# Optimization experiments

Hardware: AMD Instinct MI355X
Metric: run time of the kernel (lower is better)

Reference implementation:

```python
import jax, jax.numpy as jnp
import numpy as np

B, S, H, P, D = 4, 2048, 2048, 4096, 1024
I = min(1024, P)  # intermediate_dim


def setup_inputs() -> dict:
    key = jax.random.key(0)
    ks = jax.random.split(key, 8)
    sc = lambda n: 1.0 / np.sqrt(n)
    return {
        "x": jax.random.normal(ks[0], (B, S, H), jnp.float32),
        "tensor_pool": jax.random.normal(ks[1], (P, D), jnp.float32),
        "top_k": 2,
        "w1": jax.random.normal(ks[2], (H, I), jnp.float32) * sc(H),
        "b1": jnp.zeros((I,), jnp.float32),
        "w2": jax.random.normal(ks[3], (I, P), jnp.float32) * sc(I),
        "b2": jnp.zeros((P,), jnp.float32),
        "temperature": jnp.float32(0.5),
        "wp": jax.random.normal(ks[4], (H, D), jnp.float32) * sc(H),
        "bp": jnp.zeros((D,), jnp.float32),
        "gamma": jnp.ones((D,), jnp.float32),
        "beta": jnp.zeros((D,), jnp.float32),
        "wm": jax.random.normal(ks[5], (2 * D, D), jnp.float32) * sc(2 * D),
        "bm": jnp.zeros((D,), jnp.float32),
    }


def _layer_norm(h, gamma, beta, eps=1e-5):
    mu = jnp.mean(h, axis=-1, keepdims=True)
    var = jnp.mean(jnp.square(h - mu), axis=-1, keepdims=True)
    return (h - mu) * jax.lax.rsqrt(var + eps) * gamma + beta


def reference(x, tensor_pool, top_k, w1, b1, w2, b2, temperature, wp, bp, gamma, beta, wm, bm):
    pool_size = tensor_pool.shape[0]
    # router MLP
    inter = jax.nn.relu(jnp.einsum('bsh,hi->bsi', x, w1) + b1)
    logits = jnp.einsum('bsi,ip->bsp', inter, w2) + b2
    temp = jnp.clip(temperature, 0.1, 5.0)
    scaled_logits = jnp.clip(logits / temp, -10.0, 10.0)
    # top-k select + softmax over selected
    topk_logits, topk_idx = jax.lax.top_k(scaled_logits, top_k)  # [B,S,K]
    topk_w = jax.nn.softmax(topk_logits, axis=-1)
    # gather pool entries and combine
    experts_out = tensor_pool[topk_idx]                     # [B,S,K,D]
    weighted_map = jnp.einsum('bsk,bskd->bsd', topk_w, experts_out)
    projected_x = _layer_norm(jnp.einsum('bsh,hd->bsd', x, wp) + bp, gamma, beta)
    combined = jnp.concatenate([projected_x, weighted_map], axis=-1)  # [B,S,2D]
    transformation = jnp.einsum('bse,ed->bsd', combined, wm) + bm
    # usage stats via scatter-add
    usage = jnp.zeros((pool_size,), x.dtype).at[topk_idx.reshape(-1)].add(topk_w.reshape(-1))
    usage_fraction = usage / (usage.sum() + 1e-8)
    uniform = 1.0 / pool_size
    scale = min(1.0, x.size / (pool_size * top_k))
    diversity_loss = jnp.mean(jnp.square(usage_fraction - uniform)) * scale * 0.01
    return transformation, diversity_loss
```

## Files before the change

### kernel.cpp

```cpp
#include <hip/hip_runtime.h>
#include <hip/hip_bf16.h>
#include <float.h>
#include <limits.h>

#define NTOK 8192
#define H_   2048
#define P_   4096
#define D_   1024
#define I_   1024

#define MAXC  16
#define DELTA 0.09375f
#define TAU   4.0e-4f
#define FLAGCAP 512

typedef unsigned short ushort_t;
typedef __attribute__((ext_vector_type(8))) short short8;
typedef __attribute__((ext_vector_type(4))) float floatx4;

static __device__ inline ushort_t f2bf(float f) {
    __hip_bfloat16 h = __float2bfloat16(f);
    return *reinterpret_cast<ushort_t*>(&h);
}
static __device__ inline short f2bfs(float f) {
    __hip_bfloat16 h = __float2bfloat16(f);
    return *reinterpret_cast<short*>(&h);
}
static __device__ inline float bf2f(ushort_t s) { return __uint_as_float((unsigned)s << 16); }

static __device__ inline void ins2(float& v0, int& i0, float& v1, int& i1, float v, int i) {
    if (v > v0 || (v == v0 && i < i0)) { v1 = v0; i1 = i0; v0 = v; i0 = i; }
    else if (v > v1 || (v == v1 && i < i1)) { v1 = v; i1 = i; }
}

static __device__ __forceinline__ void gload16(const void* g, void* l) {
    __builtin_amdgcn_global_load_lds(
        (const __attribute__((address_space(1))) unsigned int*)g,
        (__attribute__((address_space(3))) unsigned int*)l,
        16, 0, 0);
}

__global__ __launch_bounds__(256) void prep_weights(
    const float* __restrict__ w2, float* __restrict__ w2tf, ushort_t* __restrict__ w2t,
    const float* __restrict__ wp, ushort_t* __restrict__ wpt,
    const float* __restrict__ wm, ushort_t* __restrict__ wmt,
    const float* __restrict__ w1, ushort_t* __restrict__ w1tHi, ushort_t* __restrict__ w1tLo)
{
    __shared__ float tile[32][33];
    const int tid = threadIdx.x;
    const int tx = tid & 31, ty = tid >> 5;
    int b = blockIdx.x;
    const float* in; int R, Cc, seg, bx, by;
    if (b < 4096)      { seg = 0; in = w2; R = I_; Cc = P_; bx = b & 127; by = b >> 7; }
    else if (b < 6144) { seg = 1; b -= 4096; in = wp; R = H_; Cc = D_; bx = b & 31; by = b >> 5; }
    else if (b < 8192) { seg = 2; b -= 6144; in = wm; R = H_; Cc = D_; bx = b & 31; by = b >> 5; }
    else               { seg = 3; b -= 8192; in = w1; R = H_; Cc = I_; bx = b & 31; by = b >> 5; }
    const int c0 = bx * 32, r0 = by * 32;
#pragma unroll
    for (int j = 0; j < 4; j++)
        tile[ty + j * 8][tx] = in[(size_t)(r0 + ty + j * 8) * Cc + c0 + tx];
    __syncthreads();
#pragma unroll
    for (int j = 0; j < 4; j++) {
        float v = tile[tx][ty + j * 8];
        const size_t o = (size_t)(c0 + ty + j * 8) * R + r0 + tx;
        if (seg == 0)      { w2t[o] = f2bf(v); w2tf[o] = v; }
        else if (seg == 1) { wpt[o] = f2bf(v); }
        else if (seg == 2) { wmt[o] = f2bf(v); }
        else { ushort_t h = f2bf(v); w1tHi[o] = h; w1tLo[o] = f2bf(v - bf2f(h)); }
    }
}

template<int ASRC, int EPI>
__global__ __launch_bounds__(256) void gemm_lds(
    const void* __restrict__ Av, int lda,
    const ushort_t* __restrict__ Bt, int ldb,
    const float* __restrict__ bias,
    float* __restrict__ Cf, ushort_t* __restrict__ Cb, int ldc, int K)
{
    __shared__ ushort_t sA[128 * 32];
    __shared__ ushort_t sB[128 * 32];

    const int tid  = threadIdx.x;
    const int wave = tid >> 6, lane = tid & 63;
    const int lr = lane & 15, lq = lane >> 4;

    const int nwg = gridDim.x * gridDim.y;
    int bid = blockIdx.y * gridDim.x + blockIdx.x;
    bid = (bid & 7) * (nwg >> 3) + (bid >> 3);
    const int bx = bid % gridDim.x, by = bid / gridDim.x;
    const int m0 = by * 128, n0 = bx * 128;
    const int m0w = m0 + (wave >> 1) * 64, n0w = n0 + (wave & 1) * 64;

    const int n1 = tid, n2 = tid + 256;

    floatx4 acc[4][4] = {};

    for (int k0 = 0; k0 < K; k0 += 32) {
        __syncthreads();
        gload16(Bt + (size_t)(n0 + (n1 >> 2)) * ldb + k0 + (n1 & 3) * 8, &sB[n1 * 8]);
        gload16(Bt + (size_t)(n0 + (n2 >> 2)) * ldb + k0 + (n2 & 3) * 8, &sB[n2 * 8]);
        if (ASRC == 1) {
            const ushort_t* Ab = (const ushort_t*)Av;
            gload16(Ab + (size_t)(m0 + (n1 >> 2)) * lda + k0 + (n1 & 3) * 8, &sA[n1 * 8]);
            gload16(Ab + (size_t)(m0 + (n2 >> 2)) * lda + k0 + (n2 & 3) * 8, &sA[n2 * 8]);
        } else {
#pragma unroll
            for (int ss = 0; ss < 2; ss++) {
                const int s = tid + ss * 256;
                const float* ap = (const float*)Av + (size_t)(m0 + (s >> 2)) * lda + k0 + (s & 3) * 8;
                float4 v0 = *(const float4*)ap;
                float4 v1 = *(const float4*)(ap + 4);
                short8 h;
                h[0] = f2bfs(v0.x); h[1] = f2bfs(v0.y); h[2] = f2bfs(v0.z); h[3] = f2bfs(v0.w);
                h[4] = f2bfs(v1.x); h[5] = f2bfs(v1.y); h[6] = f2bfs(v1.z); h[7] = f2bfs(v1.w);
                *(short8*)&sA[s * 8] = h;
            }
        }
        __syncthreads();

        short8 aF[4], bF[4];
#pragma unroll
        for (int f = 0; f < 4; f++) {
            const int ra = ((wave >> 1) * 64 + f * 16 + lr) * 32 + lq * 8;
            aF[f] = *(const short8*)&sA[ra];
            const int rb = ((wave & 1) * 64 + f * 16 + lr) * 32 + lq * 8;
            bF[f] = *(const short8*)&sB[rb];
        }
#pragma unroll
        for (int i = 0; i < 4; i++)
#pragma unroll
            for (int j = 0; j < 4; j++)
                acc[i][j] = __builtin_amdgcn_mfma_f32_16x16x32_bf16(aF[i], bF[j], acc[i][j], 0, 0, 0);
    }

#pragma unroll
    for (int j = 0; j < 4; j++) {
        const int col = n0w + j * 16 + lr;
        const float bv = bias[col];
#pragma unroll
        for (int i = 0; i < 4; i++) {
            const int rowb = m0w + i * 16 + lq * 4;
#pragma unroll
            for (int r = 0; r < 4; r++) {
                float v = acc[i][j][r] + bv;
                if (EPI == 1) Cb[(size_t)(rowb + r) * ldc + col] = f2bf(v);
                else          Cf[(size_t)(rowb + r) * ldc + col] = v;
            }
        }
    }
}

__global__ __launch_bounds__(256) void gemm_lds_split(
    const float* __restrict__ A, int lda,
    const ushort_t* __restrict__ BtH, const ushort_t* __restrict__ BtL, int ldb,
    const float* __restrict__ bias,
    float* __restrict__ Cf, ushort_t* __restrict__ Cb, int ldc, int K)
{
    __shared__ ushort_t sAh[128 * 32];
    __shared__ ushort_t sAl[128 * 32];
    __shared__ ushort_t sBh[128 * 32];
    __shared__ ushort_t sBl[128 * 32];

    const int tid  = threadIdx.x;
    const int wave = tid >> 6, lane = tid & 63;
    const int lr = lane & 15, lq = lane >> 4;

    const int nwg = gridDim.x * gridDim.y;
    int bid = blockIdx.y * gridDim.x + blockIdx.x;
    bid = (bid & 7) * (nwg >> 3) + (bid >> 3);
    const int bx = bid % gridDim.x, by = bid / gridDim.x;
    const int m0 = by * 128, n0 = bx * 128;
    const int m0w = m0 + (wave >> 1) * 64, n0w = n0 + (wave & 1) * 64;

    const int n1 = tid, n2 = tid + 256;

    floatx4 acc[4][4] = {};

    for (int k0 = 0; k0 < K; k0 += 32) {
        __syncthreads();
        gload16(BtH + (size_t)(n0 + (n1 >> 2)) * ldb + k0 + (n1 & 3) * 8, &sBh[n1 * 8]);
        gload16(BtH + (size_t)(n0 + (n2 >> 2)) * ldb + k0 + (n2 & 3) * 8, &sBh[n2 * 8]);
        gload16(BtL + (size_t)(n0 + (n1 >> 2)) * ldb + k0 + (n1 & 3) * 8, &sBl[n1 * 8]);
        gload16(BtL + (size_t)(n0 + (n2 >> 2)) * ldb + k0 + (n2 & 3) * 8, &sBl[n2 * 8]);
#pragma unroll
        for (int ss = 0; ss < 2; ss++) {
            const int s = tid + ss * 256;
            const float* ap = A + (size_t)(m0 + (s >> 2)) * lda + k0 + (s & 3) * 8;
            float4 v0 = *(const float4*)ap;
            float4 v1 = *(const float4*)(ap + 4);
            float fb[8] = {v0.x, v0.y, v0.z, v0.w, v1.x, v1.y, v1.z, v1.w};
            short8 h, l;
#pragma unroll
            for (int e = 0; e < 8; e++) {
                short hh = f2bfs(fb[e]);
                h[e] = hh; l[e] = f2bfs(fb[e] - bf2f((ushort_t)hh));
            }
            *(short8*)&sAh[s * 8] = h;
            *(short8*)&sAl[s * 8] = l;
        }
        __syncthreads();

        short8 aH[4], aL[4], bH[4], bL[4];
#pragma unroll
        for (int f = 0; f < 4; f++) {
            const int ra = ((wave >> 1) * 64 + f * 16 + lr) * 32 + lq * 8;
            aH[f] = *(const short8*)&sAh[ra];
            aL[f] = *(const short8*)&sAl[ra];
            const int rb = ((wave & 1) * 64 + f * 16 + lr) * 32 + lq * 8;
            bH[f] = *(const short8*)&sBh[rb];
            bL[f] = *(const short8*)&sBl[rb];
        }
#pragma unroll
        for (int i = 0; i < 4; i++)
#pragma unroll
            for (int j = 0; j < 4; j++) {
                acc[i][j] = __builtin_amdgcn_mfma_f32_16x16x32_bf16(aH[i], bH[j], acc[i][j], 0, 0, 0);
                acc[i][j] = __builtin_amdgcn_mfma_f32_16x16x32_bf16(aH[i], bL[j], acc[i][j], 0, 0, 0);
                acc[i][j] = __builtin_amdgcn_mfma_f32_16x16x32_bf16(aL[i], bH[j], acc[i][j], 0, 0, 0);
            }
    }

#pragma unroll
    for (int j = 0; j < 4; j++) {
        const int col = n0w + j * 16 + lr;
        const float bv = bias[col];
#pragma unroll
        for (int i = 0; i < 4; i++) {
            const int rowb = m0w + i * 16 + lq * 4;
#pragma unroll
            for (int r = 0; r < 4; r++) {
                float v = fmaxf(acc[i][j][r] + bv, 0.f);
                Cf[(size_t)(rowb + r) * ldc + col] = v;
                Cb[(size_t)(rowb + r) * ldc + col] = f2bf(v);
            }
        }
    }
}

__global__ __launch_bounds__(256) void cand_scan(
    const ushort_t* __restrict__ logitsb,
    int* __restrict__ cidx, int* __restrict__ ccnt)
{
    __shared__ float sv0[4], sv1[4];
    __shared__ int   scnt;
    const int tok = blockIdx.x;
    const int tid = threadIdx.x;
    const ushort_t* row = logitsb + (size_t)tok * P_;

    float my[16];
    {
        const uint4* rp = (const uint4*)(row + tid * 16);
        uint4 u0 = rp[0], u1 = rp[1];
        unsigned w[8] = {u0.x, u0.y, u0.z, u0.w, u1.x, u1.y, u1.z, u1.w};
#pragma unroll
        for (int j = 0; j < 8; j++) {
            my[2 * j]     = __uint_as_float(w[j] << 16);
            my[2 * j + 1] = __uint_as_float(w[j] & 0xFFFF0000u);
        }
    }
    float v0 = -FLT_MAX, v1 = -FLT_MAX;
#pragma unroll
    for (int j = 0; j < 16; j++) {
        float v = my[j];
        if (v > v0) { v1 = v0; v0 = v; } else if (v > v1) v1 = v;
    }
#pragma unroll
    for (int off = 1; off < 64; off <<= 1) {
        float u0 = __shfl_xor(v0, off), u1 = __shfl_xor(v1, off);
        float n0 = fmaxf(v0, u0);
        float n1 = fmaxf(fminf(v0, u0), fmaxf(v1, u1));
        v0 = n0; v1 = n1;
    }
    const int wv = tid >> 6;
    if ((tid & 63) == 0) { sv0[wv] = v0; sv1[wv] = v1; }
    if (tid == 0) scnt = 0;
    __syncthreads();
    float g0 = -FLT_MAX, g1 = -FLT_MAX;
#pragma unroll
    for (int w = 0; w < 4; w++) {
        float u0 = sv0[w], u1 = sv1[w];
        float n0 = fmaxf(g0, u0);
        float n1 = fmaxf(fminf(g0, u0), fmaxf(g1, u1));
        g0 = n0; g1 = n1;
    }
    const float thresh = g1 - DELTA;
#pragma unroll
    for (int j = 0; j < 16; j++) {
        if (my[j] >= thresh) {
            int pos = atomicAdd(&scnt, 1);
            if (pos < MAXC) cidx[tok * MAXC + pos] = tid * 16 + j;
        }
    }
    __syncthreads();
    if (tid == 0) ccnt[tok] = min(scnt, MAXC);
}

__global__ __launch_bounds__(256) void recheck(
    const float* __restrict__ interf, const float* __restrict__ w2tf,
    const float* __restrict__ b2, const int* __restrict__ cidx,
    const int* __restrict__ ccnt, const float* __restrict__ temp_p,
    int2* __restrict__ tki, float2* __restrict__ tkw,
    int* __restrict__ flagcnt, int* __restrict__ flaglist)
{
    __shared__ double ex[MAXC];
    __shared__ int    sidx[MAXC];
    const int tok  = blockIdx.x;
    const int tid  = threadIdx.x;
    const int wave = tid >> 6, lane = tid & 63;
    int cnt = min(max(ccnt[tok], 0), MAXC);

    const float* ir = interf + (size_t)tok * I_;
    for (int c = wave; c < cnt; c += 4) {
        int p = min(max(cidx[tok * MAXC + c], 0), P_ - 1);
        const float* wr = w2tf + (size_t)p * I_;
        double s = 0.0;
        for (int k = lane; k < I_; k += 64)
            s += (double)ir[k] * (double)wr[k];
#pragma unroll
        for (int off = 32; off; off >>= 1) s += __shfl_down(s, off);
        if (lane == 0) { ex[c] = s + (double)b2[p]; sidx[c] = p; }
    }
    __syncthreads();
    if (tid == 0) {
        float v0 = -FLT_MAX, v1 = -FLT_MAX; int i0 = INT_MAX, i1 = INT_MAX;
        for (int c = 0; c < cnt; c++) ins2(v0, i0, v1, i1, (float)ex[c], sidx[c]);
        if (i0 == INT_MAX) { i0 = 0; v0 = 0.f; }
        if (i1 == INT_MAX) { i1 = i0; v1 = v0; }
        if (cnt >= 3) {
            float v2 = -FLT_MAX;
            for (int c = 0; c < cnt; c++) {
                if (sidx[c] == i0 || sidx[c] == i1) continue;
                float v = (float)ex[c];
                if (v > v2) v2 = v;
            }
            if (v1 - v2 < TAU) {
                int pos = atomicAdd(flagcnt, 1);
                if (pos < FLAGCAP) flaglist[pos] = tok;
            }
        }
        float tc = fminf(fmaxf(temp_p[0], 0.1f), 5.0f);
        float s0 = fminf(fmaxf(v0 / tc, -10.f), 10.f);
        float s1 = fminf(fmaxf(v1 / tc, -10.f), 10.f);
        float m  = fmaxf(s0, s1);
        float e0 = expf(s0 - m), e1 = expf(s1 - m);
        float inv = 1.0f / (e0 + e1);
        tki[tok] = make_int2(i0, i1);
        tkw[tok] = make_float2(e0 * inv, e1 * inv);
    }
}

__global__ __launch_bounds__(256) void fallback_gemv(
    const float* __restrict__ x, const float* __restrict__ w1,
    const int* __restrict__ flagcnt, const int* __restrict__ flaglist,
    double* __restrict__ part)
{
    __shared__ float sx[128];
    const int tid = threadIdx.x;
    const int nf = min(flagcnt[0], FLAGCAP);
    const int nitems = nf * 16;

    for (int idx = blockIdx.x; idx < nitems; idx += gridDim.x) {
        const int fi = idx >> 4, slice = idx & 15;
        const int tok = flaglist[fi];
        const int h0 = slice * 128;
        __syncthreads();
        if (tid < 128) sx[tid] = x[(size_t)tok * H_ + h0 + tid];
        __syncthreads();

        const int col = tid * 4;
        double a0 = 0.0, a1 = 0.0, a2 = 0.0, a3 = 0.0;
        for (int h = 0; h < 128; h += 8) {
            float4 wv[8];
#pragma unroll
            for (int u = 0; u < 8; u++)
                wv[u] = *(const float4*)(w1 + (size_t)(h0 + h + u) * I_ + col);
#pragma unroll
            for (int u = 0; u < 8; u++) {
                const double xv = (double)sx[h + u];
                a0 += xv * (double)wv[u].x;
                a1 += xv * (double)wv[u].y;
                a2 += xv * (double)wv[u].z;
                a3 += xv * (double)wv[u].w;
            }
        }
        double* pp = part + ((size_t)fi * 16 + slice) * I_ + col;
        pp[0] = a0; pp[1] = a1; pp[2] = a2; pp[3] = a3;
    }
}

__global__ __launch_bounds__(256) void fallback_reduce(
    const double* __restrict__ part, const float* __restrict__ b1,
    const float* __restrict__ w2tf, const float* __restrict__ b2,
    const int* __restrict__ cidx, const int* __restrict__ ccnt,
    const int* __restrict__ flagcnt, const int* __restrict__ flaglist,
    const float* __restrict__ temp_p,
    int2* __restrict__ tki, float2* __restrict__ tkw)
{
    __shared__ double sInter[I_];
    __shared__ double ex[MAXC];
    __shared__ int    sidx[MAXC];
    const int tid  = threadIdx.x;
    const int wave = tid >> 6, lane = tid & 63;
    const int nf = min(flagcnt[0], FLAGCAP);

    for (int fi = blockIdx.x; fi < nf; fi += gridDim.x) {
        const int tok = flaglist[fi];
        __syncthreads();
#pragma unroll
        for (int q = 0; q < 4; q++) {
            const int i = q * 256 + tid;
            double v = (double)b1[i];
            const double* pp = part + (size_t)fi * 16 * I_ + i;
#pragma unroll
            for (int s = 0; s < 16; s++) v += pp[(size_t)s * I_];
            sInter[i] = v > 0.0 ? v : 0.0;
        }
        __syncthreads();

        const int cnt = min(max(ccnt[tok], 0), MAXC);
        for (int c = wave; c < cnt; c += 4) {
            int p = min(max(cidx[tok * MAXC + c], 0), P_ - 1);
            const float* wr = w2tf + (size_t)p * I_;
            double s = 0.0;
            for (int k = lane; k < I_; k += 64)
                s += sInter[k] * (double)wr[k];
#pragma unroll
            for (int off = 32; off; off >>= 1) s += __shfl_down(s, off);
            if (lane == 0) { ex[c] = s + (double)b2[p]; sidx[c] = p; }
        }
        __syncthreads();
        if (tid == 0) {
            float v0 = -FLT_MAX, v1 = -FLT_MAX; int i0 = INT_MAX, i1 = INT_MAX;
            for (int c = 0; c < cnt; c++) ins2(v0, i0, v1, i1, (float)ex[c], sidx[c]);
            if (i0 == INT_MAX) { i0 = 0; v0 = 0.f; }
            if (i1 == INT_MAX) { i1 = i0; v1 = v0; }
            float tc = fminf(fmaxf(temp_p[0], 0.1f), 5.0f);
            float s0 = fminf(fmaxf(v0 / tc, -10.f), 10.f);
            float s1 = fminf(fmaxf(v1 / tc, -10.f), 10.f);
            float m  = fmaxf(s0, s1);
            float e0 = expf(s0 - m), e1 = expf(s1 - m);
            float inv = 1.0f / (e0 + e1);
            tki[tok] = make_int2(i0, i1);
            tkw[tok] = make_float2(e0 * inv, e1 * inv);
        }
    }
}

static __device__ inline float blockReduceSum256(float v, float* red) {
#pragma unroll
    for (int off = 32; off; off >>= 1) v += __shfl_down(v, off);
    const int wv = threadIdx.x >> 6;
    if ((threadIdx.x & 63) == 0) red[wv] = v;
    __syncthreads();
    float tot = red[0] + red[1] + red[2] + red[3];
    __syncthreads();
    return tot;
}

__global__ __launch_bounds__(256) void build_combined(
    const float* __restrict__ proj, ushort_t* __restrict__ comb,
    const float* __restrict__ pool,
    const float* __restrict__ gamma, const float* __restrict__ beta,
    const int2* __restrict__ tki, const float2* __restrict__ tkw,
    float* __restrict__ usage)
{
    __shared__ float red[4];
    const int tok = blockIdx.x;
    const int tid = threadIdx.x;
    const int c = tid * 4;

    float4 v = *(const float4*)&proj[(size_t)tok * D_ + c];
    float s = v.x + v.y + v.z + v.w;
    float tot = blockReduceSum256(s, red);
    float mu = tot * (1.0f / D_);
    float d0 = v.x - mu, d1 = v.y - mu, d2 = v.z - mu, d3 = v.w - mu;
    float sq = d0 * d0 + d1 * d1 + d2 * d2 + d3 * d3;
    float var = blockReduceSum256(sq, red) * (1.0f / D_);
    float rs = 1.0f / sqrtf(var + 1e-5f);

    float4 g  = *(const float4*)&gamma[c];
    float4 be = *(const float4*)&beta[c];
    ushort4 o;
    o.x = f2bf(d0 * rs * g.x + be.x);
    o.y = f2bf(d1 * rs * g.y + be.y);
    o.z = f2bf(d2 * rs * g.z + be.z);
    o.w = f2bf(d3 * rs * g.w + be.w);
    *(ushort4*)&comb[(size_t)tok * (2 * D_) + c] = o;

    int2   ii = tki[tok];
    int ia = min(max(ii.x, 0), P_ - 1);
    int ib = min(max(ii.y, 0), P_ - 1);
    float2 ww = tkw[tok];
    float4 p0 = *(const float4*)&pool[(size_t)ia * D_ + c];
    float4 p1 = *(const float4*)&pool[(size_t)ib * D_ + c];
    ushort4 wm;
    wm.x = f2bf(ww.x * p0.x + ww.y * p1.x);
    wm.y = f2bf(ww.x * p0.y + ww.y * p1.y);
    wm.z = f2bf(ww.x * p0.z + ww.y * p1.z);
    wm.w = f2bf(ww.x * p0.w + ww.y * p1.w);
    *(ushort4*)&comb[(size_t)tok * (2 * D_) + D_ + c] = wm;

    if (tid == 0) {
        atomicAdd(&usage[ia], ww.x);
        atomicAdd(&usage[ib], ww.y);
    }
}

__global__ __launch_bounds__(256) void diversity_kernel(
    const float* __restrict__ usage, float* __restrict__ out)
{
    __shared__ float red[4];
    const int tid = threadIdx.x;
    float s = 0.f;
    for (int j = tid; j < P_; j += 256) s += usage[j];
    float tot = blockReduceSum256(s, red) + 1e-8f;
    float q = 0.f;
    const float uni = 1.0f / P_;
    for (int j = tid; j < P_; j += 256) {
        float f = usage[j] / tot - uni;
        q += f * f;
    }
    float ssq = blockReduceSum256(q, red);
    if (tid == 0) out[(size_t)NTOK * D_] = ssq * (1.0f / P_) * 0.01f;
}

extern "C" void kernel_launch(void* const* d_in, const int* in_sizes, int n_in,
                              void* d_out, int out_size, void* d_ws, size_t ws_size,
                              hipStream_t stream) {
    const float* x     = (const float*)d_in[0];
    const float* pool  = (const float*)d_in[1];
    const float* w1    = (const float*)d_in[3];
    const float* b1    = (const float*)d_in[4];
    const float* w2    = (const float*)d_in[5];
    const float* b2    = (const float*)d_in[6];
    const float* temp  = (const float*)d_in[7];
    const float* wp    = (const float*)d_in[8];
    const float* bp    = (const float*)d_in[9];
    const float* gamma = (const float*)d_in[10];
    const float* beta  = (const float*)d_in[11];
    const float* wm    = (const float*)d_in[12];
    const float* bm    = (const float*)d_in[13];
    float* out = (float*)d_out;

    float* ws = (float*)d_ws;
    const size_t MF = (size_t)1024 * 1024;
    float*    interf  = ws;
    ushort_t* interb  = (ushort_t*)(ws + 8 * MF);
    ushort_t* logitsb = (ushort_t*)(ws + 12 * MF);
    double*   part    = (double*)(ws + 12 * MF);
    float*    projb   = ws + 12 * MF;
    ushort_t* comb    = (ushort_t*)(ws + 20 * MF);
    float*    w2tf    = ws + 28 * MF;
    ushort_t* w2t     = (ushort_t*)(ws + 32 * MF);
    ushort_t* wpt     = (ushort_t*)(ws + 34 * MF);
    ushort_t* wmt     = (ushort_t*)(ws + 35 * MF);
    ushort_t* w1tHi   = (ushort_t*)(ws + 36 * MF);
    ushort_t* w1tLo   = (ushort_t*)(ws + 37 * MF);
    int*      cidx    = (int*)(ws + 38 * MF);
    int*      ccnt    = cidx + NTOK * MAXC;
    int2*     tki     = (int2*)(ccnt + NTOK);
    float2*   tkw     = (float2*)(tki + NTOK);
    float*    usage   = (float*)(tkw + NTOK);
    int*      flagcnt = (int*)(usage + P_);
    int*      flaglist= flagcnt + 1;

    hipMemsetAsync(usage, 0, (P_ + 1) * sizeof(float), stream);

    dim3 blk(256);
    prep_weights<<<10240, blk, 0, stream>>>(w2, w2tf, w2t, wp, wpt, wm, wmt,
                                            w1, w1tHi, w1tLo);

    gemm_lds_split<<<dim3(I_ / 128, NTOK / 128), blk, 0, stream>>>(
        x, H_, w1tHi, w1tLo, H_, b1, interf, interb, I_, H_);

    gemm_lds<1, 1><<<dim3(P_ / 128, NTOK / 128), blk, 0, stream>>>(
        interb, I_, w2t, I_, b2, nullptr, logitsb, P_, I_);

    cand_scan<<<NTOK, blk, 0, stream>>>(logitsb, cidx, ccnt);
    recheck<<<NTOK, blk, 0, stream>>>(interf, w2tf, b2, cidx, ccnt, temp, tki, tkw,
                                      flagcnt, flaglist);

    fallback_gemv<<<1024, blk, 0, stream>>>(x, w1, flagcnt, flaglist, part);
    fallback_reduce<<<128, blk, 0, stream>>>(part, b1, w2tf, b2, cidx, ccnt,
                                             flagcnt, flaglist, temp, tki, tkw);

    gemm_lds<0, 0><<<dim3(D_ / 128, NTOK / 128), blk, 0, stream>>>(
        x, H_, wpt, H_, bp, projb, nullptr, D_, H_);

    build_combined<<<NTOK, blk, 0, stream>>>(projb, comb, pool, gamma, beta, tki, tkw, usage);

    gemm_lds<1, 0><<<dim3(D_ / 128, NTOK / 128), blk, 0, stream>>>(
        comb, 2 * D_, wmt, 2 * D_, bm, out, nullptr, D_, H_);

    diversity_kernel<<<1, blk, 0, stream>>>(usage, out);
}
```

Baseline: 592.9 us.

## Add 256x256 triple-buffered pipelined bf16 GEMM for logits and merge GEMMs

Adds a new 512-thread GEMM kernel with 256x256 tiles and three LDS buffers. Each k-step prefetches two steps ahead through direct global-to-LDS loads, uses an XOR-swizzled LDS layout, and raises wave priority around the MFMA blocks. The router logits GEMM and the final merge GEMM now use it, aiming for more reuse per tile and better overlap of loads with compute. The trade-off is a larger LDS footprint and more register pressure, plus fewer workgroups for the D-wide GEMM (128 blocks).

```diff
diff --git a/kernel.cpp b/kernel.cpp
--- a/kernel.cpp
+++ b/kernel.cpp
@@ -68,6 +68,115 @@
         else if (seg == 1) { wpt[o] = f2bf(v); }
         else if (seg == 2) { wmt[o] = f2bf(v); }
         else { ushort_t h = f2bf(v); w1tHi[o] = h; w1tLo[o] = f2bf(v - bf2f(h)); }
+    }
+}
+
+static __device__ __forceinline__ void stage_u(
+    const ushort_t* __restrict__ base, int ld, int r0, int kt, int u, int tid,
+    ushort_t* __restrict__ lds)
+{
+    const int p = u * 512 + tid;
+    const int row = p >> 2;
+    const int chunk = (p ^ (p >> 2)) & 3;
+    gload16(base + (size_t)(r0 + row) * ld + kt * 32 + chunk * 8, lds + p * 8);
+}
+
+template<int EPI>
+__global__ __launch_bounds__(512, 2) void gemm_pipe256(
+    const ushort_t* __restrict__ A, int lda,
+    const ushort_t* __restrict__ Bt, int ldb,
+    const float* __restrict__ bias,
+    float* __restrict__ Cf, ushort_t* __restrict__ Cb, int ldc, int K)
+{
+    __shared__ ushort_t sA[3][256 * 32];
+    __shared__ ushort_t sB[3][256 * 32];
+
+    const int tid  = threadIdx.x;
+    const int wave = tid >> 6, lane = tid & 63;
+    const int lr = lane & 15, lq = lane >> 4;
+    const int wm = wave >> 2, wn = wave & 3;
+
+    const int nwg = gridDim.x * gridDim.y;
+    int bid = blockIdx.y * gridDim.x + blockIdx.x;
+    bid = (bid & 7) * (nwg >> 3) + (bid >> 3);
+    const int bx = bid % gridDim.x, by = bid / gridDim.x;
+    const int m0 = by * 256, n0 = bx * 256;
+    const int NT = K >> 5;
+
+    floatx4 acc[8][4] = {};
+
+#pragma unroll
+    for (int u = 0; u < 2; u++) stage_u(A,  lda, m0, 0, u, tid, &sA[0][0]);
+#pragma unroll
+    for (int u = 0; u < 2; u++) stage_u(Bt, ldb, n0, 0, u, tid, &sB[0][0]);
+#pragma unroll
+    for (int u = 0; u < 2; u++) stage_u(A,  lda, m0, 1, u, tid, &sA[1][0]);
+#pragma unroll
+    for (int u = 0; u < 2; u++) stage_u(Bt, ldb, n0, 1, u, tid, &sB[1][0]);
+
+    for (int kt = 0; kt < NT; kt++) {
+        const int cb = kt % 3;
+        const int sbuf = (kt + 2) % 3;
+        const bool st = (kt + 2) < NT;
+        const ushort_t* __restrict__ sAc = &sA[cb][0];
+        const ushort_t* __restrict__ sBc = &sB[cb][0];
+        short8 bF[4];
+
+#pragma unroll
+        for (int p = 0; p < 4; p++) {
+            if (p == 0) {
+                if (kt + 1 < NT) asm volatile("s_waitcnt vmcnt(4)" ::: "memory");
+                else             asm volatile("s_waitcnt vmcnt(0)" ::: "memory");
+                __builtin_amdgcn_s_barrier();
+            } else {
+                __builtin_amdgcn_s_barrier();
+            }
+            short8 aF[2];
+#pragma unroll
+            for (int t = 0; t < 2; t++) {
+                const int row = wm * 128 + (2 * p + t) * 16 + lr;
+                const int ph = row * 4 + (lq ^ (row & 3));
+                aF[t] = *(const short8*)&sAc[ph * 8];
+            }
+            if (p == 0) {
+#pragma unroll
+                for (int f = 0; f < 4; f++) {
+                    const int row = wn * 64 + f * 16 + lr;
+                    const int ph = row * 4 + (lq ^ (row & 3));
+                    bF[f] = *(const short8*)&sBc[ph * 8];
+                }
+            }
+            if (st) {
+                if (p == 0)      stage_u(A,  lda, m0, kt + 2, 0, tid, &sA[sbuf][0]);
+                else if (p == 1) stage_u(A,  lda, m0, kt + 2, 1, tid, &sA[sbuf][0]);
+                else if (p == 2) stage_u(Bt, ldb, n0, kt + 2, 0, tid, &sB[sbuf][0]);
+                else             stage_u(Bt, ldb, n0, kt + 2, 1, tid, &sB[sbuf][0]);
+            }
+            __builtin_amdgcn_s_setprio(1);
+#pragma unroll
+            for (int t = 0; t < 2; t++)
+#pragma unroll
+                for (int j = 0; j < 4; j++)
+                    acc[2 * p + t][j] = __builtin_amdgcn_mfma_f32_16x16x32_bf16(
+                        aF[t], bF[j], acc[2 * p + t][j], 0, 0, 0);
+            __builtin_amdgcn_s_setprio(0);
+        }
+    }
+
+#pragma unroll
+    for (int j = 0; j < 4; j++) {
+        const int col = n0 + wn * 64 + j * 16 + lr;
+        const float bv = bias[col];
+#pragma unroll
+        for (int i = 0; i < 8; i++) {
+            const int rowb = m0 + wm * 128 + i * 16 + lq * 4;
+#pragma unroll
+            for (int r = 0; r < 4; r++) {
+                float v = acc[i][j][r] + bv;
+                if (EPI == 1) Cb[(size_t)(rowb + r) * ldc + col] = f2bf(v);
+                else          Cf[(size_t)(rowb + r) * ldc + col] = v;
+            }
+        }
     }
 }
 
@@ -574,7 +683,7 @@
     gemm_lds_split<<<dim3(I_ / 128, NTOK / 128), blk, 0, stream>>>(
         x, H_, w1tHi, w1tLo, H_, b1, interf, interb, I_, H_);
 
-    gemm_lds<1, 1><<<dim3(P_ / 128, NTOK / 128), blk, 0, stream>>>(
+    gemm_pipe256<1><<<dim3(P_ / 256, NTOK / 256), dim3(512), 0, stream>>>(
         interb, I_, w2t, I_, b2, nullptr, logitsb, P_, I_);
 
     cand_scan<<<NTOK, blk, 0, stream>>>(logitsb, cidx, ccnt);
@@ -590,8 +699,8 @@
 
     build_combined<<<NTOK, blk, 0, stream>>>(projb, comb, pool, gamma, beta, tki, tkw, usage);
 
-    gemm_lds<1, 0><<<dim3(D_ / 128, NTOK / 128), blk, 0, stream>>>(
-        comb, 2 * D_, wmt, 2 * D_, bm, out, nullptr, D_, H_);
+    gemm_pipe256<0><<<dim3(D_ / 256, NTOK / 256), dim3(512), 0, stream>>>(
+        comb, 2 * D_, wmt, 2 * D_, bm, out, nullptr, D_, 2 * D_);
 
     diversity_kernel<<<1, blk, 0, stream>>>(usage, out);
 }
```

After: 624.7 us. 1.05x slower.
